# Kernel tuning notes

Measured on AMD Instinct MI355X. Metric: run time of the kernel, lower is better.

Reference implementation:

```python
import jax, jax.numpy as jnp
import numpy as np

B, H, T, D = 4, 16, 2048, 128

def setup_inputs() -> dict:
    key = jax.random.key(0)
    kq, kk, kv = jax.random.split(key, 3)
    q = jax.random.normal(kq, (B, H, T, D), dtype=jnp.float32)
    k = jax.random.normal(kk, (B, H, T, D), dtype=jnp.float32)
    v = jax.random.normal(kv, (B, H, T, D), dtype=jnp.float32)
    return {"q": q, "k": k, "v": v}

def reference(q, k, v):
    # scores: [B,H,T,T] = q @ k^T, masked multiplicatively by causal lower-tri ones
    T_ = q.shape[-2]
    mask = jnp.tril(jnp.ones((T_, T_), dtype=q.dtype))  # CausalMulMask
    scores = jnp.einsum('bhid,bhjd->bhij', q, k) * mask
    # no softmax: linear attention, scores @ v
    return jnp.einsum('bhij,bhjd->bhid', scores, v)
```

## Files before the change

kernel.cpp:

```cpp
#include <hip/hip_runtime.h>
#include <stdint.h>

#define SEQ    2048
#define DIM    128
#define CHUNK  128
#define NCHUNK 16
#define NBH    64
#define RECSH  16384

typedef __attribute__((ext_vector_type(8))) short short8;
typedef __attribute__((ext_vector_type(4))) float floatx4;

#define MFMA(a, b, c) __builtin_amdgcn_mfma_f32_16x16x32_bf16((a), (b), (c), 0, 0, 0)

__device__ __forceinline__ short f2bf(float f) {
  union { float f; uint32_t u; } x; x.f = f;
  uint32_t r = x.u + 0x7fffu + ((x.u >> 16) & 1u);
  return (short)(r >> 16);
}
__device__ __forceinline__ float bf2f(short s) {
  union { uint32_t u; float f; } x;
  x.u = ((uint32_t)(uint16_t)s) << 16;
  return x.f;
}
__device__ __forceinline__ short8 pack8(const float4 a, const float4 b) {
  short8 s;
  s[0] = f2bf(a.x); s[1] = f2bf(a.y); s[2] = f2bf(a.z); s[3] = f2bf(a.w);
  s[4] = f2bf(b.x); s[5] = f2bf(b.y); s[6] = f2bf(b.z); s[7] = f2bf(b.w);
  return s;
}
__device__ __forceinline__ void gload16(const void* g, void* l) {
  __builtin_amdgcn_global_load_lds(
      (const __attribute__((address_space(1))) void*)g,
      (__attribute__((address_space(3))) void*)l, 16, 0, 0);
}

__global__ __launch_bounds__(512, 2) void k_cstate(
    const float* __restrict__ kin, const float* __restrict__ vin,
    short* __restrict__ ws) {
  const int blk = blockIdx.x;
  const int bh  = blk & 63;
  const int c   = blk >> 6;
  const size_t base = (size_t)bh * SEQ * DIM + (size_t)c * CHUNK * DIM;
  const float* kc = kin + base;
  const float* vc = vin + base;

  __shared__ short Kt[128][136];
  __shared__ short Vt[128][136];

  const int tid  = threadIdx.x;
  const int wave = tid >> 6;
  const int lane = tid & 63;
  const int q4   = lane >> 4;
  const int l16  = lane & 15;
  const int j    = tid & 127;
  const int dhi  = tid >> 7;

#pragma unroll
  for (int it = 0; it < 4; ++it) {
    const int d0 = it * 32 + dhi * 8;
    const float* krow = kc + (size_t)j * DIM + d0;
    const float4 ka = *(const float4*)krow;
    const float4 kb2 = *(const float4*)(krow + 4);
    Kt[d0 + 0][j] = f2bf(ka.x); Kt[d0 + 1][j] = f2bf(ka.y);
    Kt[d0 + 2][j] = f2bf(ka.z); Kt[d0 + 3][j] = f2bf(ka.w);
    Kt[d0 + 4][j] = f2bf(kb2.x); Kt[d0 + 5][j] = f2bf(kb2.y);
    Kt[d0 + 6][j] = f2bf(kb2.z); Kt[d0 + 7][j] = f2bf(kb2.w);
    const float* vrow = vc + (size_t)j * DIM + d0;
    const float4 va = *(const float4*)vrow;
    const float4 vb2 = *(const float4*)(vrow + 4);
    Vt[d0 + 0][j] = f2bf(va.x); Vt[d0 + 1][j] = f2bf(va.y);
    Vt[d0 + 2][j] = f2bf(va.z); Vt[d0 + 3][j] = f2bf(va.w);
    Vt[d0 + 4][j] = f2bf(vb2.x); Vt[d0 + 5][j] = f2bf(vb2.y);
    Vt[d0 + 6][j] = f2bf(vb2.z); Vt[d0 + 7][j] = f2bf(vb2.w);
  }
  __syncthreads();

  floatx4 acc[8];
#pragma unroll
  for (int m = 0; m < 8; ++m)
#pragma unroll
    for (int r = 0; r < 4; ++r) acc[m][r] = 0.f;
#pragma unroll
  for (int ks = 0; ks < 4; ++ks) {
    const short8 bk = *(const short8*)&Kt[wave * 16 + l16][ks * 32 + q4 * 8];
#pragma unroll
    for (int m = 0; m < 8; ++m) {
      const short8 av = *(const short8*)&Vt[m * 16 + l16][ks * 32 + q4 * 8];
      acc[m] = MFMA(av, bk, acc[m]);
    }
  }
  __syncthreads();

  short (*Ss)[136] = (short (*)[136])Kt;
#pragma unroll
  for (int m = 0; m < 8; ++m)
#pragma unroll
    for (int r = 0; r < 4; ++r)
      Ss[m * 16 + q4 * 4 + r][wave * 16 + l16] = f2bf(acc[m][r]);
  __syncthreads();

  short* rec = ws + (size_t)(bh * NCHUNK + c) * RECSH;
#pragma unroll
  for (int i = 0; i < 4; ++i) {
    const int t8  = i * 512 + tid;
    const int row = ((t8 >> 9) << 5) + (((t8 >> 6) & 1) << 4) + (t8 & 15);
    const int col = (((t8 >> 7) & 3) << 5) + (((t8 >> 4) & 3) << 3);
    *(short8*)&rec[(size_t)t8 * 8] = *(const short8*)&Ss[row][col];
  }
}

__global__ __launch_bounds__(256, 4) void k_prefix(short* __restrict__ ws) {
  const int blk = blockIdx.x;
  const int bh  = blk & 63;
  const int p   = blk >> 6;
  const int off = p * 2048 + threadIdx.x * 8;
  short* wb = ws + (size_t)bh * NCHUNK * RECSH;

  float run[8];
#pragma unroll
  for (int s = 0; s < 8; ++s) run[s] = 0.f;
#pragma unroll
  for (int cc = 0; cc < NCHUNK; ++cc) {
    short8* ptr = (short8*)&wb[(size_t)cc * RECSH + off];
    const short8 rv = *ptr;
    short8 ov;
#pragma unroll
    for (int s = 0; s < 8; ++s) ov[s] = f2bf(run[s]);
    *ptr = ov;
#pragma unroll
    for (int s = 0; s < 8; ++s) run[s] += bf2f(rv[s]);
  }
}

__global__ __launch_bounds__(512, 2) void k_out(
    const float* __restrict__ qin, const float* __restrict__ kin,
    const float* __restrict__ vin, const short* __restrict__ ws,
    float* __restrict__ out) {
  const int blk = blockIdx.x;
  const int bh  = blk & 63;
  const int c   = blk >> 6;
  const size_t base = (size_t)bh * SEQ * DIM + (size_t)c * CHUNK * DIM;
  const float* qc = qin + base;
  const float* kc = kin + base;
  const float* vc = vin + base;
  float* oc = out + base;

  __shared__ short Klds[128][136];
  __shared__ short Vt[128][136];
  __shared__ short Ps[128][136];
  __shared__ __align__(16) short Sb[RECSH];

  const int tid  = threadIdx.x;
  const int wave = tid >> 6;
  const int lane = tid & 63;
  const int q4   = lane >> 4;
  const int l16  = lane & 15;
  const int j    = tid & 127;
  const int dhi  = tid >> 7;

  const short* sp = ws + (size_t)(bh * NCHUNK + c) * RECSH;
#pragma unroll
  for (int i = 0; i < 4; ++i) {
    const int g = i * 512 + tid;
    gload16(&sp[(size_t)g * 8], &Sb[(size_t)g * 8]);
  }

  const float* qrow = qc + (size_t)(wave * 16 + l16) * DIM + q4 * 8;
  short8 aq[4];
#pragma unroll
  for (int ks = 0; ks < 4; ++ks)
    aq[ks] = pack8(*(const float4*)(qrow + ks * 32),
                   *(const float4*)(qrow + ks * 32 + 4));

#pragma unroll
  for (int it = 0; it < 4; ++it) {
    const int e = it * 4096 + tid * 8;
    *(short8*)&Klds[e >> 7][e & 127] =
        pack8(*(const float4*)(kc + e), *(const float4*)(kc + e + 4));
  }
#pragma unroll
  for (int it = 0; it < 4; ++it) {
    const int d0 = it * 32 + dhi * 8;
    const float* vrow = vc + (size_t)j * DIM + d0;
    const float4 a = *(const float4*)vrow;
    const float4 b = *(const float4*)(vrow + 4);
    Vt[d0 + 0][j] = f2bf(a.x); Vt[d0 + 1][j] = f2bf(a.y);
    Vt[d0 + 2][j] = f2bf(a.z); Vt[d0 + 3][j] = f2bf(a.w);
    Vt[d0 + 4][j] = f2bf(b.x); Vt[d0 + 5][j] = f2bf(b.y);
    Vt[d0 + 6][j] = f2bf(b.z); Vt[d0 + 7][j] = f2bf(b.w);
  }
  __syncthreads();

  floatx4 oacc[8];
#pragma unroll
  for (int tn = 0; tn < 8; ++tn)
#pragma unroll
    for (int r = 0; r < 4; ++r) oacc[tn][r] = 0.f;

#pragma unroll
  for (int ks = 0; ks < 4; ++ks)
#pragma unroll
    for (int tn = 0; tn < 8; ++tn) {
      const short8 bs = *(const short8*)
          &Sb[(tn >> 1) * 4096 + ks * 1024 + (tn & 1) * 512 + lane * 8];
      oacc[tn] = MFMA(aq[ks], bs, oacc[tn]);
    }

  for (int tj = 0; tj <= wave; ++tj) {
    floatx4 sacc;
#pragma unroll
    for (int r = 0; r < 4; ++r) sacc[r] = 0.f;
#pragma unroll
    for (int ks = 0; ks < 4; ++ks) {
      const short8 bk = *(const short8*)&Klds[tj * 16 + l16][ks * 32 + q4 * 8];
      sacc = MFMA(aq[ks], bk, sacc);
    }
#pragma unroll
    for (int r = 0; r < 4; ++r) {
      float val = sacc[r];
      if (tj == wave && l16 > q4 * 4 + r) val = 0.f;
      Ps[wave * 16 + q4 * 4 + r][tj * 16 + l16] = f2bf(val);
    }
  }
  if ((wave & 1) == 0) {
#pragma unroll
    for (int r = 0; r < 4; ++r)
      Ps[wave * 16 + q4 * 4 + r][(wave + 1) * 16 + l16] = 0;
  }

  const int kst = (wave + 2) >> 1;
  for (int t = 0; t < kst; ++t) {
    const short8 ap = *(const short8*)&Ps[wave * 16 + l16][t * 32 + q4 * 8];
#pragma unroll
    for (int tn = 0; tn < 8; ++tn) {
      const short8 bv = *(const short8*)&Vt[tn * 16 + l16][t * 32 + q4 * 8];
      oacc[tn] = MFMA(ap, bv, oacc[tn]);
    }
  }

#pragma unroll
  for (int tn = 0; tn < 8; ++tn)
#pragma unroll
    for (int r = 0; r < 4; ++r)
      oc[(size_t)(wave * 16 + q4 * 4 + r) * DIM + tn * 16 + l16] = oacc[tn][r];
}

extern "C" void kernel_launch(void* const* d_in, const int* in_sizes, int n_in,
                              void* d_out, int out_size, void* d_ws, size_t ws_size,
                              hipStream_t stream) {
  const float* q = (const float*)d_in[0];
  const float* k = (const float*)d_in[1];
  const float* v = (const float*)d_in[2];
  float* out = (float*)d_out;
  (void)in_sizes; (void)n_in; (void)out_size; (void)ws_size;
  short* ws = (short*)d_ws;

  hipLaunchKernelGGL(k_cstate, dim3(NBH * NCHUNK), dim3(512), 0, stream,
                     k, v, ws);
  hipLaunchKernelGGL(k_prefix, dim3(NBH * 8), dim3(256), 0, stream, ws);
  hipLaunchKernelGGL(k_out, dim3(NBH * NCHUNK), dim3(512), 0, stream,
                     q, k, v, ws, out);
}
```

Before: 275.9 us.

## Stage bf16 K/V chunks in output buffer and bulk-load them into swizzled LDS

```diff
diff --git a/kernel.cpp b/kernel.cpp
--- a/kernel.cpp
+++ b/kernel.cpp
@@ -7,6 +7,7 @@
 #define NCHUNK 16
 #define NBH    64
 #define RECSH  16384
+#define KVSH   32768
 
 typedef __attribute__((ext_vector_type(8))) short short8;
 typedef __attribute__((ext_vector_type(4))) float floatx4;
@@ -34,16 +35,20 @@
       (const __attribute__((address_space(1))) void*)g,
       (__attribute__((address_space(3))) void*)l, 16, 0, 0);
 }
+__device__ __forceinline__ int swz(int row, int colsh) {
+  return row * 128 + (colsh ^ ((row & 7) << 3));
+}
 
 __global__ __launch_bounds__(512, 2) void k_cstate(
     const float* __restrict__ kin, const float* __restrict__ vin,
-    short* __restrict__ ws) {
+    short* __restrict__ ws, short* outw) {
   const int blk = blockIdx.x;
   const int bh  = blk & 63;
   const int c   = blk >> 6;
   const size_t base = (size_t)bh * SEQ * DIM + (size_t)c * CHUNK * DIM;
   const float* kc = kin + base;
   const float* vc = vin + base;
+  short* rec = outw + (size_t)(bh * NCHUNK + c) * KVSH;
 
   __shared__ short Kt[128][136];
   __shared__ short Vt[128][136];
@@ -66,6 +71,7 @@
     Kt[d0 + 2][j] = f2bf(ka.z); Kt[d0 + 3][j] = f2bf(ka.w);
     Kt[d0 + 4][j] = f2bf(kb2.x); Kt[d0 + 5][j] = f2bf(kb2.y);
     Kt[d0 + 6][j] = f2bf(kb2.z); Kt[d0 + 7][j] = f2bf(kb2.w);
+    *(short8*)&rec[swz(j, d0)] = pack8(ka, kb2);
     const float* vrow = vc + (size_t)j * DIM + d0;
     const float4 va = *(const float4*)vrow;
     const float4 vb2 = *(const float4*)(vrow + 4);
@@ -76,6 +82,13 @@
   }
   __syncthreads();
 
+#pragma unroll
+  for (int i = 0; i < 4; ++i) {
+    const int g = i * 512 + tid;
+    const int r = g >> 4, cg = g & 15;
+    *(short8*)&rec[16384 + swz(r, cg * 8)] = *(const short8*)&Vt[r][cg * 8];
+  }
+
   floatx4 acc[8];
 #pragma unroll
   for (int m = 0; m < 8; ++m)
@@ -100,13 +113,13 @@
       Ss[m * 16 + q4 * 4 + r][wave * 16 + l16] = f2bf(acc[m][r]);
   __syncthreads();
 
-  short* rec = ws + (size_t)(bh * NCHUNK + c) * RECSH;
+  short* srec = ws + (size_t)(bh * NCHUNK + c) * RECSH;
 #pragma unroll
   for (int i = 0; i < 4; ++i) {
     const int t8  = i * 512 + tid;
     const int row = ((t8 >> 9) << 5) + (((t8 >> 6) & 1) << 4) + (t8 & 15);
     const int col = (((t8 >> 7) & 3) << 5) + (((t8 >> 4) & 3) << 3);
-    *(short8*)&rec[(size_t)t8 * 8] = *(const short8*)&Ss[row][col];
+    *(short8*)&srec[(size_t)t8 * 8] = *(const short8*)&Ss[row][col];
   }
 }
 
@@ -134,36 +147,34 @@
 }
 
 __global__ __launch_bounds__(512, 2) void k_out(
-    const float* __restrict__ qin, const float* __restrict__ kin,
-    const float* __restrict__ vin, const short* __restrict__ ws,
-    float* __restrict__ out) {
+    const float* __restrict__ qin, const short* __restrict__ ws,
+    float* out) {
   const int blk = blockIdx.x;
   const int bh  = blk & 63;
   const int c   = blk >> 6;
   const size_t base = (size_t)bh * SEQ * DIM + (size_t)c * CHUNK * DIM;
   const float* qc = qin + base;
-  const float* kc = kin + base;
-  const float* vc = vin + base;
   float* oc = out + base;
-
-  __shared__ short Klds[128][136];
-  __shared__ short Vt[128][136];
-  __shared__ short Ps[128][136];
-  __shared__ __align__(16) short Sb[RECSH];
+  const short* rec = (const short*)out + (size_t)(bh * NCHUNK + c) * KVSH;
+
+  __shared__ __align__(16) short KVS[49152];
 
   const int tid  = threadIdx.x;
   const int wave = tid >> 6;
   const int lane = tid & 63;
   const int q4   = lane >> 4;
   const int l16  = lane & 15;
-  const int j    = tid & 127;
-  const int dhi  = tid >> 7;
-
+
+#pragma unroll
+  for (int i = 0; i < 8; ++i) {
+    const int g = i * 512 + tid;
+    gload16(&rec[(size_t)g * 8], &KVS[(size_t)g * 8]);
+  }
   const short* sp = ws + (size_t)(bh * NCHUNK + c) * RECSH;
 #pragma unroll
   for (int i = 0; i < 4; ++i) {
     const int g = i * 512 + tid;
-    gload16(&sp[(size_t)g * 8], &Sb[(size_t)g * 8]);
+    gload16(&sp[(size_t)g * 8], &KVS[32768 + (size_t)g * 8]);
   }
 
   const float* qrow = qc + (size_t)(wave * 16 + l16) * DIM + q4 * 8;
@@ -172,24 +183,6 @@
   for (int ks = 0; ks < 4; ++ks)
     aq[ks] = pack8(*(const float4*)(qrow + ks * 32),
                    *(const float4*)(qrow + ks * 32 + 4));
-
-#pragma unroll
-  for (int it = 0; it < 4; ++it) {
-    const int e = it * 4096 + tid * 8;
-    *(short8*)&Klds[e >> 7][e & 127] =
-        pack8(*(const float4*)(kc + e), *(const float4*)(kc + e + 4));
-  }
-#pragma unroll
-  for (int it = 0; it < 4; ++it) {
-    const int d0 = it * 32 + dhi * 8;
-    const float* vrow = vc + (size_t)j * DIM + d0;
-    const float4 a = *(const float4*)vrow;
-    const float4 b = *(const float4*)(vrow + 4);
-    Vt[d0 + 0][j] = f2bf(a.x); Vt[d0 + 1][j] = f2bf(a.y);
-    Vt[d0 + 2][j] = f2bf(a.z); Vt[d0 + 3][j] = f2bf(a.w);
-    Vt[d0 + 4][j] = f2bf(b.x); Vt[d0 + 5][j] = f2bf(b.y);
-    Vt[d0 + 6][j] = f2bf(b.z); Vt[d0 + 7][j] = f2bf(b.w);
-  }
   __syncthreads();
 
   floatx4 oacc[8];
@@ -203,38 +196,49 @@
 #pragma unroll
     for (int tn = 0; tn < 8; ++tn) {
       const short8 bs = *(const short8*)
-          &Sb[(tn >> 1) * 4096 + ks * 1024 + (tn & 1) * 512 + lane * 8];
+          &KVS[32768 + (tn >> 1) * 4096 + ks * 1024 + (tn & 1) * 512 + lane * 8];
       oacc[tn] = MFMA(aq[ks], bs, oacc[tn]);
     }
 
-  for (int tj = 0; tj <= wave; ++tj) {
-    floatx4 sacc;
-#pragma unroll
-    for (int r = 0; r < 4; ++r) sacc[r] = 0.f;
+  floatx4 sacc[8];
+#pragma unroll
+  for (int tj = 0; tj < 8; ++tj) {
+    if (tj > wave) continue;
+#pragma unroll
+    for (int r = 0; r < 4; ++r) sacc[tj][r] = 0.f;
 #pragma unroll
     for (int ks = 0; ks < 4; ++ks) {
-      const short8 bk = *(const short8*)&Klds[tj * 16 + l16][ks * 32 + q4 * 8];
-      sacc = MFMA(aq[ks], bk, sacc);
-    }
+      const short8 bk =
+          *(const short8*)&KVS[swz(tj * 16 + l16, ks * 32 + q4 * 8)];
+      sacc[tj] = MFMA(aq[ks], bk, sacc[tj]);
+    }
+  }
+  __syncthreads();
+
+#pragma unroll
+  for (int tj = 0; tj < 8; ++tj) {
+    if (tj > wave) continue;
 #pragma unroll
     for (int r = 0; r < 4; ++r) {
-      float val = sacc[r];
+      float val = sacc[tj][r];
       if (tj == wave && l16 > q4 * 4 + r) val = 0.f;
-      Ps[wave * 16 + q4 * 4 + r][tj * 16 + l16] = f2bf(val);
+      KVS[swz(wave * 16 + q4 * 4 + r, tj * 16 + l16)] = f2bf(val);
     }
   }
   if ((wave & 1) == 0) {
 #pragma unroll
     for (int r = 0; r < 4; ++r)
-      Ps[wave * 16 + q4 * 4 + r][(wave + 1) * 16 + l16] = 0;
+      KVS[swz(wave * 16 + q4 * 4 + r, (wave + 1) * 16 + l16)] = 0;
   }
 
   const int kst = (wave + 2) >> 1;
   for (int t = 0; t < kst; ++t) {
-    const short8 ap = *(const short8*)&Ps[wave * 16 + l16][t * 32 + q4 * 8];
+    const short8 ap =
+        *(const short8*)&KVS[swz(wave * 16 + l16, t * 32 + q4 * 8)];
 #pragma unroll
     for (int tn = 0; tn < 8; ++tn) {
-      const short8 bv = *(const short8*)&Vt[tn * 16 + l16][t * 32 + q4 * 8];
+      const short8 bv =
+          *(const short8*)&KVS[16384 + swz(tn * 16 + l16, t * 32 + q4 * 8)];
       oacc[tn] = MFMA(ap, bv, oacc[tn]);
     }
   }
@@ -257,8 +261,8 @@
   short* ws = (short*)d_ws;
 
   hipLaunchKernelGGL(k_cstate, dim3(NBH * NCHUNK), dim3(512), 0, stream,
-                     k, v, ws);
+                     k, v, ws, (short*)d_out);
   hipLaunchKernelGGL(k_prefix, dim3(NBH * 8), dim3(256), 0, stream, ws);
   hipLaunchKernelGGL(k_out, dim3(NBH * NCHUNK), dim3(512), 0, stream,
-                     q, k, v, ws, out);
-}
+                     q, ws, out);
+}
```

After: 283.4 us. +2.7%, slower.
